# Kernel optimization log

Measured on AMD Instinct MI355X. Metric: run time of the kernel, lower is better.

## Reference

```python
import jax, jax.numpy as jnp
import numpy as np

EPS = 1e-16
S = 20  # amino-acid alphabet size, hardcoded in original (reshape to (-1,20,20))


def make_rate_matrix(R, p):
    """R: (n,S,S) symmetric, zero diag; p: (n,S) equilibrium. Returns normalized Q: (n,S,S)."""
    Q = R * p[:, None, :]
    diag = jnp.sum(Q, axis=-1, keepdims=True)          # (n,S,1)
    Q = Q - diag * jnp.eye(S, dtype=p.dtype)           # put -rowsum on diagonal
    mue = jnp.sum(p[..., None] * diag, axis=-2, keepdims=True)  # (n,1,1) expected mutation rate
    return Q / jnp.maximum(mue, EPS)


def setup_inputs() -> dict:
    key = jax.random.key(0)
    k1, k2, k3, k4, k5 = jax.random.split(key, 5)
    m, b, L, k, num_rates = 2, 512, 512, 2, 512
    sequences = jax.random.randint(k1, (m, b, L), 0, S, dtype=jnp.int32)
    rate_indices = jax.random.randint(k2, (m, b), 0, num_rates, dtype=jnp.int32)
    tau_kernel = jax.random.normal(k3, (m, num_rates), dtype=jnp.float32) - 3.0  # rate_init = const(-3)
    exchangeability_kernel = jax.random.normal(k4, (m, k, S, S), dtype=jnp.float32)
    equilibrium_kernel = jax.random.normal(k5, (m, k, S), dtype=jnp.float32)
    return {"sequences": sequences, "rate_indices": rate_indices, "tau_kernel": tau_kernel,
            "exchangeability_kernel": exchangeability_kernel, "equilibrium_kernel": equilibrium_kernel}


def reference(sequences, rate_indices, tau_kernel, exchangeability_kernel, equilibrium_kernel):
    m, k = exchangeability_kernel.shape[:2]
    b = sequences.shape[1]
    # make_R: symmetrize, softplus, zero diagonal
    R = jax.nn.softplus(0.5 * (exchangeability_kernel + jnp.swapaxes(exchangeability_kernel, -1, -2)))
    R = R * (1.0 - jnp.eye(S, dtype=R.dtype))
    # make_p: softmax equilibrium
    p = jax.nn.softmax(equilibrium_kernel, axis=-1)
    # normalized rate matrices Q: (m,k,S,S)
    Q = make_rate_matrix(R.reshape(-1, S, S), p.reshape(-1, S)).reshape(m, k, S, S)
    # make_tau: gather per-sequence time, softplus
    tau = jax.nn.softplus(tau_kernel[jnp.arange(m)[:, None], rate_indices])  # (m,b)
    # tau*Q and batched matrix exponential: (m,b,k,S,S)
    tauQ = tau[:, :, None, None, None] * Q[:, None]
    P = jax.scipy.linalg.expm(tauQ)
    # embedding-lookup combine: ancprobs[m,b,l,k,:] = P[m,b,k,seq[m,b,l],:]
    P_t = jnp.transpose(P, (0, 1, 3, 2, 4))  # (m,b,S,k,S)
    mi = jnp.arange(m)[:, None, None]
    bi = jnp.arange(b)[None, :, None]
    ancprobs = P_t[mi, bi, sequences]  # (m,b,L,k,S)
    return ancprobs
```

## Files before the change

kernel.cpp:

```cpp
#include <hip/hip_runtime.h>
#include <math.h>

#define SA 20
#define KDIM 2
#define MDIM 2
#define BDIM 512
#define LDIM 512
#define NRATES 512
#define PPB 4
#define THREADS 256
#define NCH (LDIM * KDIM * SA / 4)

__device__ __forceinline__ float softplusf(float x) {
    return fmaxf(x, 0.0f) + log1pf(expf(-fabsf(x)));
}

__device__ __forceinline__ void mmB(float* C, const float* A, const float* Bl) {
    #pragma unroll
    for (int j = 0; j < SA; ++j) C[j] = 0.0f;
    #pragma unroll
    for (int t = 0; t < SA; ++t) {
        const float a = A[t];
        const float4* row = reinterpret_cast<const float4*>(Bl + t * SA);
        #pragma unroll
        for (int q = 0; q < 5; ++q) {
            float4 b = row[q];
            C[4*q+0] = fmaf(a, b.x, C[4*q+0]);
            C[4*q+1] = fmaf(a, b.y, C[4*q+1]);
            C[4*q+2] = fmaf(a, b.z, C[4*q+2]);
            C[4*q+3] = fmaf(a, b.w, C[4*q+3]);
        }
    }
}

__device__ __forceinline__ void stageRow(float* dst, const float* T, int row, bool act) {
    if (act) {
        float4* d4 = reinterpret_cast<float4*>(dst + row * SA);
        #pragma unroll
        for (int q = 0; q < 5; ++q)
            d4[q] = make_float4(T[4*q+0], T[4*q+1], T[4*q+2], T[4*q+3]);
    }
}

__global__ __launch_bounds__(THREADS) void ancprobs_fused_kernel(
    const int*   __restrict__ seqg,
    const int*   __restrict__ rateIdx,
    const float* __restrict__ tauk,
    const float* __restrict__ Ek,
    const float* __restrict__ eqk,
    float*       __restrict__ out)
{
    __shared__ float sP[PPB * KDIM * SA * SA];
    __shared__ int   sSeq[PPB * LDIM];

    const int tid  = threadIdx.x;
    const int w    = tid >> 6;
    const int lane = tid & 63;
    const int mb   = blockIdx.x * PPB + w;
    const int mm   = mb >> 9;

    {
        const int4* sq = reinterpret_cast<const int4*>(seqg + (size_t)mb * LDIM);
        int4* dst = reinterpret_cast<int4*>(sSeq + w * LDIM);
        dst[lane]      = sq[lane];
        dst[lane + 64] = sq[lane + 64];
    }

    const int  half = lane >> 5;
    const int  row  = lane & 31;
    const bool act  = row < SA;
    const int  mk   = mm * KDIM + half;
    float* stage = sP + (w * KDIM + half) * SA * SA;

    float e = act ? eqk[mk * SA + row] : -INFINITY;
    float mx = e;
    #pragma unroll
    for (int off = 16; off; off >>= 1) mx = fmaxf(mx, __shfl_xor(mx, off, 32));
    float ex = act ? expf(e - mx) : 0.0f;
    float sm = ex;
    #pragma unroll
    for (int off = 16; off; off >>= 1) sm += __shfl_xor(sm, off, 32);
    float p_i = ex / sm;

    const int r0 = act ? row : 0;
    float A[SA];
    float dg = 0.0f;
    #pragma unroll
    for (int j = 0; j < SA; ++j) {
        float pj = __shfl(p_i, j, 32);
        float e1 = Ek[(mk * SA + r0) * SA + j];
        float e2 = Ek[(mk * SA + j) * SA + r0];
        float r  = (j == row) ? 0.0f : softplusf(0.5f * (e1 + e2));
        float q  = r * pj;
        A[j] = q;
        dg  += q;
    }
    float t_ = act ? p_i * dg : 0.0f;
    #pragma unroll
    for (int off = 16; off; off >>= 1) t_ += __shfl_xor(t_, off, 32);
    const float inv = 1.0f / fmaxf(t_, 1e-16f);

    const float tau = softplusf(tauk[mm * NRATES + rateIdx[mb]]);
    const float sc  = tau * inv;
    #pragma unroll
    for (int j = 0; j < SA; ++j)
        A[j] = act ? ((j == row) ? -dg * sc : A[j] * sc) : 0.0f;

    float rn = 0.0f;
    #pragma unroll
    for (int j = 0; j < SA; ++j) rn += fabsf(A[j]);
    #pragma unroll
    for (int off = 16; off; off >>= 1) rn = fmaxf(rn, __shfl_xor(rn, off, 32));
    int s = 0;
    if (rn > 1.0f) s = (int)ceilf(log2f(rn));
    if (s < 0) s = 0;
    if (s > 30) s = 30;
    const float scale = exp2f((float)(-s));
    #pragma unroll
    for (int j = 0; j < SA; ++j) A[j] *= scale;
    const int smax = max(s, __shfl_xor(s, 32, 64));

    float A2[SA], A3[SA], T[SA];
    stageRow(stage, A, row, act);
    mmB(A2, A, stage);
    mmB(A3, A2, stage);
    #pragma unroll
    for (int j = 0; j < SA; ++j) {
        float id = (j == row) ? 1.0f : 0.0f;
        T[j] = (1.0f/6.0f)*id + (1.0f/24.0f)*A[j] + (1.0f/120.0f)*A2[j] + (1.0f/720.0f)*A3[j];
    }
    stageRow(stage, T, row, act);
    {
        float P1[SA];
        mmB(P1, A3, stage);
        #pragma unroll
        for (int j = 0; j < SA; ++j) {
            float id = (j == row) ? 1.0f : 0.0f;
            T[j] = P1[j] + id + A[j] + 0.5f * A2[j];
        }
    }
    for (int it = 0; it < smax; ++it) {
        stageRow(stage, T, row, act);
        float Tn[SA];
        mmB(Tn, T, stage);
        const bool doit = it < s;
        #pragma unroll
        for (int j = 0; j < SA; ++j) T[j] = doit ? Tn[j] : T[j];
    }
    stageRow(stage, T, row, act);

    __syncthreads();

    const float4* pv = reinterpret_cast<const float4*>(sP);
    #pragma unroll 1
    for (int pr = 0; pr < PPB; ++pr) {
        float4* o4 = reinterpret_cast<float4*>(out) + (size_t)(blockIdx.x * PPB + pr) * NCH;
        const int* sq = sSeq + pr * LDIM;
        for (int f = tid; f < NCH; f += THREADS) {
            int l  = f / 10;
            int ch = f - l * 10;
            int kk = (ch >= 5) ? 1 : 0;
            int c4 = ch - kk * 5;
            o4[f] = pv[((pr * KDIM + kk) * SA + sq[l]) * 5 + c4];
        }
    }
}

extern "C" void kernel_launch(void* const* d_in, const int* in_sizes, int n_in,
                              void* d_out, int out_size, void* d_ws, size_t ws_size,
                              hipStream_t stream) {
    const int*   seq  = (const int*)d_in[0];
    const int*   ridx = (const int*)d_in[1];
    const float* tauk = (const float*)d_in[2];
    const float* Ek   = (const float*)d_in[3];
    const float* eqk  = (const float*)d_in[4];
    float* out = (float*)d_out;

    ancprobs_fused_kernel<<<(MDIM * BDIM) / PPB, THREADS, 0, stream>>>(
        seq, ridx, tauk, Ek, eqk, out);
}
```

Before: 109.8 us.

## Split fused kernel into expm kernel and wide gather kernel via workspace

```diff
diff --git a/kernel.cpp b/kernel.cpp
--- a/kernel.cpp
+++ b/kernel.cpp
@@ -7,9 +7,10 @@
 #define BDIM 512
 #define LDIM 512
 #define NRATES 512
-#define PPB 4
-#define THREADS 256
 #define NCH (LDIM * KDIM * SA / 4)
+#define GBLK_PER_PAIR 4
+#define GCHUNK (NCH / GBLK_PER_PAIR)
+#define GITER (GCHUNK / 256)
 
 __device__ __forceinline__ float softplusf(float x) {
     return fmaxf(x, 0.0f) + log1pf(expf(-fabsf(x)));
@@ -42,35 +43,24 @@
     }
 }
 
-__global__ __launch_bounds__(THREADS) void ancprobs_fused_kernel(
-    const int*   __restrict__ seqg,
+__global__ __launch_bounds__(64) void expm_kernel(
     const int*   __restrict__ rateIdx,
     const float* __restrict__ tauk,
     const float* __restrict__ Ek,
     const float* __restrict__ eqk,
-    float*       __restrict__ out)
+    float*       __restrict__ Pg)
 {
-    __shared__ float sP[PPB * KDIM * SA * SA];
-    __shared__ int   sSeq[PPB * LDIM];
+    __shared__ float sStage[KDIM * SA * SA];
 
-    const int tid  = threadIdx.x;
-    const int w    = tid >> 6;
-    const int lane = tid & 63;
-    const int mb   = blockIdx.x * PPB + w;
+    const int lane = threadIdx.x;
+    const int mb   = blockIdx.x;
     const int mm   = mb >> 9;
-
-    {
-        const int4* sq = reinterpret_cast<const int4*>(seqg + (size_t)mb * LDIM);
-        int4* dst = reinterpret_cast<int4*>(sSeq + w * LDIM);
-        dst[lane]      = sq[lane];
-        dst[lane + 64] = sq[lane + 64];
-    }
 
     const int  half = lane >> 5;
     const int  row  = lane & 31;
     const bool act  = row < SA;
     const int  mk   = mm * KDIM + half;
-    float* stage = sP + (w * KDIM + half) * SA * SA;
+    float* stage = sStage + half * SA * SA;
 
     float e = act ? eqk[mk * SA + row] : -INFINITY;
     float mx = e;
@@ -147,23 +137,47 @@
         #pragma unroll
         for (int j = 0; j < SA; ++j) T[j] = doit ? Tn[j] : T[j];
     }
-    stageRow(stage, T, row, act);
 
-    __syncthreads();
+    if (act) {
+        float4* d4 = reinterpret_cast<float4*>(Pg + ((size_t)mb * KDIM + half) * SA * SA + row * SA);
+        #pragma unroll
+        for (int q = 0; q < 5; ++q)
+            d4[q] = make_float4(T[4*q+0], T[4*q+1], T[4*q+2], T[4*q+3]);
+    }
+}
 
-    const float4* pv = reinterpret_cast<const float4*>(sP);
-    #pragma unroll 1
-    for (int pr = 0; pr < PPB; ++pr) {
-        float4* o4 = reinterpret_cast<float4*>(out) + (size_t)(blockIdx.x * PPB + pr) * NCH;
-        const int* sq = sSeq + pr * LDIM;
-        for (int f = tid; f < NCH; f += THREADS) {
-            int l  = f / 10;
-            int ch = f - l * 10;
-            int kk = (ch >= 5) ? 1 : 0;
-            int c4 = ch - kk * 5;
-            o4[f] = pv[((pr * KDIM + kk) * SA + sq[l]) * 5 + c4];
-        }
+__global__ __launch_bounds__(256) void gather_kernel(
+    const int*   __restrict__ seqg,
+    const float* __restrict__ Pg,
+    float*       __restrict__ out)
+{
+    const int tid   = threadIdx.x;
+    const int mb    = blockIdx.x >> 2;
+    const int cbase = (blockIdx.x & 3) * GCHUNK + tid;
+
+    const int*    sq = seqg + (size_t)mb * LDIM;
+    const float4* P4 = reinterpret_cast<const float4*>(Pg + (size_t)mb * KDIM * SA * SA);
+    float4*       o4 = reinterpret_cast<float4*>(out) + (size_t)mb * NCH;
+
+    int c[GITER], l[GITER], sqv[GITER], idx[GITER];
+    #pragma unroll
+    for (int i = 0; i < GITER; ++i) c[i] = cbase + i * 256;
+    #pragma unroll
+    for (int i = 0; i < GITER; ++i) l[i] = c[i] / 10;
+    #pragma unroll
+    for (int i = 0; i < GITER; ++i) sqv[i] = sq[l[i]];
+    #pragma unroll
+    for (int i = 0; i < GITER; ++i) {
+        int ch = c[i] - l[i] * 10;
+        int kk = (ch >= 5) ? 1 : 0;
+        int c4 = ch - kk * 5;
+        idx[i] = (kk * SA + sqv[i]) * 5 + c4;
     }
+    float4 v[GITER];
+    #pragma unroll
+    for (int i = 0; i < GITER; ++i) v[i] = P4[idx[i]];
+    #pragma unroll
+    for (int i = 0; i < GITER; ++i) o4[c[i]] = v[i];
 }
 
 extern "C" void kernel_launch(void* const* d_in, const int* in_sizes, int n_in,
@@ -175,7 +189,8 @@
     const float* Ek   = (const float*)d_in[3];
     const float* eqk  = (const float*)d_in[4];
     float* out = (float*)d_out;
+    float* Pg  = (float*)d_ws;
 
-    ancprobs_fused_kernel<<<(MDIM * BDIM) / PPB, THREADS, 0, stream>>>(
-        seq, ridx, tauk, Ek, eqk, out);
+    expm_kernel<<<MDIM * BDIM, 64, 0, stream>>>(ridx, tauk, Ek, eqk, Pg);
+    gather_kernel<<<MDIM * BDIM * GBLK_PER_PAIR, 256, 0, stream>>>(seq, Pg, out);
 }
```

New measurement: 121.0 us. 1.1x slower.

## Precompute Q powers once per model and split gather across four blocks per sequence

Applied to the files above, without the earlier changes.

```diff
diff --git a/kernel.cpp b/kernel.cpp
--- a/kernel.cpp
+++ b/kernel.cpp
@@ -7,9 +7,14 @@
 #define BDIM 512
 #define LDIM 512
 #define NRATES 512
-#define PPB 4
-#define THREADS 256
+#define NPOW 7
+#define MATW (SA * SA)
+#define PWSTRIDE (NPOW * MATW)
+#define SPLIT 4
 #define NCH (LDIM * KDIM * SA / 4)
+#define GCH (NCH / SPLIT)
+#define GITER (GCH / 256)
+#define LSLICE (LDIM / SPLIT)
 
 __device__ __forceinline__ float softplusf(float x) {
     return fmaxf(x, 0.0f) + log1pf(expf(-fabsf(x)));
@@ -42,35 +47,30 @@
     }
 }
 
-__global__ __launch_bounds__(THREADS) void ancprobs_fused_kernel(
-    const int*   __restrict__ seqg,
-    const int*   __restrict__ rateIdx,
-    const float* __restrict__ tauk,
+__device__ __forceinline__ void writeMat(float* base, const float* T, int row, bool act) {
+    if (act) {
+        float4* d4 = reinterpret_cast<float4*>(base + row * SA);
+        #pragma unroll
+        for (int q = 0; q < 5; ++q)
+            d4[q] = make_float4(T[4*q+0], T[4*q+1], T[4*q+2], T[4*q+3]);
+    }
+}
+
+__global__ __launch_bounds__(64) void powers_kernel(
     const float* __restrict__ Ek,
     const float* __restrict__ eqk,
-    float*       __restrict__ out)
+    float*       __restrict__ Pw,
+    float*       __restrict__ nInf)
 {
-    __shared__ float sP[PPB * KDIM * SA * SA];
-    __shared__ int   sSeq[PPB * LDIM];
-
-    const int tid  = threadIdx.x;
-    const int w    = tid >> 6;
-    const int lane = tid & 63;
-    const int mb   = blockIdx.x * PPB + w;
-    const int mm   = mb >> 9;
-
-    {
-        const int4* sq = reinterpret_cast<const int4*>(seqg + (size_t)mb * LDIM);
-        int4* dst = reinterpret_cast<int4*>(sSeq + w * LDIM);
-        dst[lane]      = sq[lane];
-        dst[lane + 64] = sq[lane + 64];
-    }
-
-    const int  half = lane >> 5;
-    const int  row  = lane & 31;
-    const bool act  = row < SA;
-    const int  mk   = mm * KDIM + half;
-    float* stage = sP + (w * KDIM + half) * SA * SA;
+    __shared__ float sB[KDIM * MATW];
+
+    const int lane = threadIdx.x;
+    const int mm   = blockIdx.x;
+    const int half = lane >> 5;
+    const int row  = lane & 31;
+    const bool act = row < SA;
+    const int mk   = mm * KDIM + half;
+    float* stg = sB + half * MATW;
 
     float e = act ? eqk[mk * SA + row] : -INFINITY;
     float mx = e;
@@ -83,7 +83,7 @@
     float p_i = ex / sm;
 
     const int r0 = act ? row : 0;
-    float A[SA];
+    float Q[SA];
     float dg = 0.0f;
     #pragma unroll
     for (int j = 0; j < SA; ++j) {
@@ -92,77 +92,160 @@
         float e2 = Ek[(mk * SA + j) * SA + r0];
         float r  = (j == row) ? 0.0f : softplusf(0.5f * (e1 + e2));
         float q  = r * pj;
-        A[j] = q;
+        Q[j] = q;
         dg  += q;
     }
     float t_ = act ? p_i * dg : 0.0f;
     #pragma unroll
     for (int off = 16; off; off >>= 1) t_ += __shfl_xor(t_, off, 32);
     const float inv = 1.0f / fmaxf(t_, 1e-16f);
-
-    const float tau = softplusf(tauk[mm * NRATES + rateIdx[mb]]);
-    const float sc  = tau * inv;
     #pragma unroll
     for (int j = 0; j < SA; ++j)
-        A[j] = act ? ((j == row) ? -dg * sc : A[j] * sc) : 0.0f;
+        Q[j] = act ? ((j == row) ? -dg * inv : Q[j] * inv) : 0.0f;
 
     float rn = 0.0f;
     #pragma unroll
-    for (int j = 0; j < SA; ++j) rn += fabsf(A[j]);
+    for (int j = 0; j < SA; ++j) rn += fabsf(Q[j]);
     #pragma unroll
     for (int off = 16; off; off >>= 1) rn = fmaxf(rn, __shfl_xor(rn, off, 32));
-    int s = 0;
-    if (rn > 1.0f) s = (int)ceilf(log2f(rn));
-    if (s < 0) s = 0;
-    if (s > 30) s = 30;
-    const float scale = exp2f((float)(-s));
-    #pragma unroll
-    for (int j = 0; j < SA; ++j) A[j] *= scale;
-    const int smax = max(s, __shfl_xor(s, 32, 64));
-
-    float A2[SA], A3[SA], T[SA];
-    stageRow(stage, A, row, act);
-    mmB(A2, A, stage);
-    mmB(A3, A2, stage);
-    #pragma unroll
-    for (int j = 0; j < SA; ++j) {
-        float id = (j == row) ? 1.0f : 0.0f;
-        T[j] = (1.0f/6.0f)*id + (1.0f/24.0f)*A[j] + (1.0f/120.0f)*A2[j] + (1.0f/720.0f)*A3[j];
-    }
-    stageRow(stage, T, row, act);
-    {
-        float P1[SA];
-        mmB(P1, A3, stage);
-        #pragma unroll
-        for (int j = 0; j < SA; ++j) {
-            float id = (j == row) ? 1.0f : 0.0f;
-            T[j] = P1[j] + id + A[j] + 0.5f * A2[j];
+    if (act && row == 0) nInf[mk] = rn;
+
+    float* base = Pw + (size_t)mk * PWSTRIDE;
+    if (act) {
+        float I[SA];
+        #pragma unroll
+        for (int j = 0; j < SA; ++j) I[j] = (j == row) ? 1.0f : 0.0f;
+        writeMat(base + 0 * MATW, I, row, act);
+    }
+    writeMat(base + 1 * MATW, Q, row, act);
+
+    stageRow(stg, Q, row, act);
+    __syncthreads();
+    float G2[SA], G3[SA];
+    mmB(G2, Q, stg);
+    writeMat(base + 2 * MATW, G2, row, act);
+    mmB(G3, G2, stg);
+    writeMat(base + 3 * MATW, G3, row, act);
+    __syncthreads();
+    stageRow(stg, G2, row, act);
+    __syncthreads();
+    {
+        float G4[SA];
+        mmB(G4, G2, stg);
+        writeMat(base + 4 * MATW, G4, row, act);
+    }
+    {
+        float G5[SA];
+        mmB(G5, G3, stg);
+        writeMat(base + 5 * MATW, G5, row, act);
+    }
+    __syncthreads();
+    stageRow(stg, G3, row, act);
+    __syncthreads();
+    {
+        float G6[SA];
+        mmB(G6, G3, stg);
+        writeMat(base + 6 * MATW, G6, row, act);
+    }
+}
+
+__global__ __launch_bounds__(256) void combo_gather_kernel(
+    const int*   __restrict__ seqg,
+    const int*   __restrict__ rateIdx,
+    const float* __restrict__ tauk,
+    const float* __restrict__ Pw,
+    const float* __restrict__ nInf,
+    float*       __restrict__ out)
+{
+    __shared__ float sPw[KDIM * PWSTRIDE];
+    __shared__ float sP[KDIM * MATW];
+    __shared__ int   sSeq[LSLICE];
+
+    const int tid = threadIdx.x;
+    const int mb  = blockIdx.x >> 2;
+    const int qq  = blockIdx.x & 3;
+    const int mm  = mb >> 9;
+
+    {
+        const float4* src = reinterpret_cast<const float4*>(Pw + (size_t)mm * KDIM * PWSTRIDE);
+        float4* dst = reinterpret_cast<float4*>(sPw);
+        for (int f = tid; f < KDIM * PWSTRIDE / 4; f += 256) dst[f] = src[f];
+    }
+    if (tid >= 64 && tid < 96) {
+        reinterpret_cast<int4*>(sSeq)[tid - 64] =
+            reinterpret_cast<const int4*>(seqg + (size_t)mb * LDIM)[qq * (LSLICE / 4) + (tid - 64)];
+    }
+    __syncthreads();
+
+    if (tid < 64) {
+        const int lane = tid;
+        const int half = lane >> 5;
+        const int row  = lane & 31;
+        const bool act = row < SA;
+        const int r0   = act ? row : 0;
+
+        const float tau = softplusf(tauk[mm * NRATES + rateIdx[mb]]);
+        const float n   = nInf[mm * KDIM + half];
+        float x0 = tau * n;
+        int s = 0;
+        if (x0 > 1.0f) s = (int)ceilf(log2f(x0));
+        if (s < 0) s = 0;
+        if (s > 30) s = 30;
+        const float x = tau * exp2f(-(float)s);
+
+        float cf[NPOW];
+        cf[0] = 1.0f;
+        cf[1] = x;
+        cf[2] = cf[1] * x * 0.5f;
+        cf[3] = cf[2] * x * (1.0f / 3.0f);
+        cf[4] = cf[3] * x * 0.25f;
+        cf[5] = cf[4] * x * 0.2f;
+        cf[6] = cf[5] * x * (1.0f / 6.0f);
+
+        float T[SA];
+        #pragma unroll
+        for (int j = 0; j < SA; ++j) T[j] = (j == row) ? 1.0f : 0.0f;
+        const float* pb = sPw + half * PWSTRIDE + r0 * SA;
+        #pragma unroll
+        for (int d = 1; d < NPOW; ++d) {
+            const float c = cf[d];
+            const float4* rp = reinterpret_cast<const float4*>(pb + d * MATW);
+            #pragma unroll
+            for (int q = 0; q < 5; ++q) {
+                float4 b = rp[q];
+                T[4*q+0] = fmaf(c, b.x, T[4*q+0]);
+                T[4*q+1] = fmaf(c, b.y, T[4*q+1]);
+                T[4*q+2] = fmaf(c, b.z, T[4*q+2]);
+                T[4*q+3] = fmaf(c, b.w, T[4*q+3]);
+            }
         }
-    }
-    for (int it = 0; it < smax; ++it) {
-        stageRow(stage, T, row, act);
-        float Tn[SA];
-        mmB(Tn, T, stage);
-        const bool doit = it < s;
-        #pragma unroll
-        for (int j = 0; j < SA; ++j) T[j] = doit ? Tn[j] : T[j];
-    }
-    stageRow(stage, T, row, act);
-
+
+        const int smax = max(s, __shfl_xor(s, 32));
+        float* stg = sP + half * MATW;
+        for (int it = 0; it < smax; ++it) {
+            stageRow(stg, T, row, act);
+            float Tn[SA];
+            mmB(Tn, T, stg);
+            const bool doit = it < s;
+            #pragma unroll
+            for (int j = 0; j < SA; ++j) T[j] = doit ? Tn[j] : T[j];
+        }
+        stageRow(stg, T, row, act);
+    }
     __syncthreads();
 
     const float4* pv = reinterpret_cast<const float4*>(sP);
-    #pragma unroll 1
-    for (int pr = 0; pr < PPB; ++pr) {
-        float4* o4 = reinterpret_cast<float4*>(out) + (size_t)(blockIdx.x * PPB + pr) * NCH;
-        const int* sq = sSeq + pr * LDIM;
-        for (int f = tid; f < NCH; f += THREADS) {
-            int l  = f / 10;
-            int ch = f - l * 10;
-            int kk = (ch >= 5) ? 1 : 0;
-            int c4 = ch - kk * 5;
-            o4[f] = pv[((pr * KDIM + kk) * SA + sq[l]) * 5 + c4];
-        }
+    float4* o4 = reinterpret_cast<float4*>(out) + (size_t)mb * NCH;
+    const int cb = qq * GCH + tid;
+    #pragma unroll
+    for (int i = 0; i < GITER; ++i) {
+        const int c  = cb + i * 256;
+        const int l  = c / 10;
+        const int ch = c - l * 10;
+        const int kk = (ch >= 5) ? 1 : 0;
+        const int c4 = ch - kk * 5;
+        const int sq = sSeq[l - qq * LSLICE];
+        o4[c] = pv[(kk * SA + sq) * 5 + c4];
     }
 }
 
@@ -174,8 +257,11 @@
     const float* tauk = (const float*)d_in[2];
     const float* Ek   = (const float*)d_in[3];
     const float* eqk  = (const float*)d_in[4];
-    float* out = (float*)d_out;
-
-    ancprobs_fused_kernel<<<(MDIM * BDIM) / PPB, THREADS, 0, stream>>>(
-        seq, ridx, tauk, Ek, eqk, out);
-}
+    float* out  = (float*)d_out;
+    float* Pw   = (float*)d_ws;
+    float* nInf = (float*)d_ws + MDIM * KDIM * PWSTRIDE;
+
+    powers_kernel<<<MDIM, 64, 0, stream>>>(Ek, eqk, Pw, nInf);
+    combo_gather_kernel<<<MDIM * BDIM * SPLIT, 256, 0, stream>>>(
+        seq, ridx, tauk, Pw, nInf, out);
+}
```

Measured after the change: 122.5 us. 1.12x slower.

## Precompute Q powers once per block and evaluate Taylor polynomial per tau

Applied to the files above, without the earlier changes.

```diff
diff --git a/kernel.cpp b/kernel.cpp
--- a/kernel.cpp
+++ b/kernel.cpp
@@ -7,8 +7,7 @@
 #define BDIM 512
 #define LDIM 512
 #define NRATES 512
-#define PPB 4
-#define THREADS 256
+#define MATW (SA * SA)
 #define NCH (LDIM * KDIM * SA / 4)
 
 __device__ __forceinline__ float softplusf(float x) {
@@ -42,7 +41,7 @@
     }
 }
 
-__global__ __launch_bounds__(THREADS) void ancprobs_fused_kernel(
+__global__ __launch_bounds__(256) void ancprobs_onepass_kernel(
     const int*   __restrict__ seqg,
     const int*   __restrict__ rateIdx,
     const float* __restrict__ tauk,
@@ -50,119 +49,188 @@
     const float* __restrict__ eqk,
     float*       __restrict__ out)
 {
-    __shared__ float sP[PPB * KDIM * SA * SA];
-    __shared__ int   sSeq[PPB * LDIM];
+    __shared__ __align__(16) float sPw[KDIM][6][MATW];
+    __shared__ __align__(16) float sT[2][KDIM][MATW];
+    __shared__ int   sSeq[LDIM];
+    __shared__ float sn[KDIM];
 
     const int tid  = threadIdx.x;
+    const int mb   = blockIdx.x;
+    const int mm   = mb >> 9;
     const int w    = tid >> 6;
     const int lane = tid & 63;
-    const int mb   = blockIdx.x * PPB + w;
-    const int mm   = mb >> 9;
-
+
+    const int   ri  = rateIdx[mb];
+    const float tau = softplusf(tauk[mm * NRATES + ri]);
+
+    if (tid < 128)
+        reinterpret_cast<int4*>(sSeq)[tid] =
+            reinterpret_cast<const int4*>(seqg + (size_t)mb * LDIM)[tid];
+
+    if (w == 0) {
+        const int  half = lane >> 5;
+        const int  row  = lane & 31;
+        const bool act  = row < SA;
+        const int  mk   = mm * KDIM + half;
+        const int  r0   = act ? row : 0;
+
+        float e = act ? eqk[mk * SA + row] : -INFINITY;
+        float mx = e;
+        #pragma unroll
+        for (int off = 16; off; off >>= 1) mx = fmaxf(mx, __shfl_xor(mx, off, 32));
+        float ex = act ? expf(e - mx) : 0.0f;
+        float sm = ex;
+        #pragma unroll
+        for (int off = 16; off; off >>= 1) sm += __shfl_xor(sm, off, 32);
+        float p_i = ex / sm;
+
+        float Q[SA];
+        float dg = 0.0f;
+        #pragma unroll
+        for (int j = 0; j < SA; ++j) {
+            float pj = __shfl(p_i, j, 32);
+            float e1 = Ek[(mk * SA + r0) * SA + j];
+            float e2 = Ek[(mk * SA + j) * SA + r0];
+            float r  = (j == row) ? 0.0f : softplusf(0.5f * (e1 + e2));
+            float q  = r * pj;
+            Q[j] = q;
+            dg  += q;
+        }
+        float t_ = act ? p_i * dg : 0.0f;
+        #pragma unroll
+        for (int off = 16; off; off >>= 1) t_ += __shfl_xor(t_, off, 32);
+        const float inv = 1.0f / fmaxf(t_, 1e-16f);
+        #pragma unroll
+        for (int j = 0; j < SA; ++j)
+            Q[j] = act ? ((j == row) ? -dg * inv : Q[j] * inv) : 0.0f;
+
+        float rn = 0.0f;
+        #pragma unroll
+        for (int j = 0; j < SA; ++j) rn += fabsf(Q[j]);
+        #pragma unroll
+        for (int off = 16; off; off >>= 1) rn = fmaxf(rn, __shfl_xor(rn, off, 32));
+        if (act && row == 0) sn[half] = rn;
+
+        stageRow(&sPw[half][0][0], Q, row, act);
+        float G2[SA];
+        mmB(G2, Q, &sPw[half][0][0]);
+        stageRow(&sPw[half][1][0], G2, row, act);
+        float G3[SA];
+        mmB(G3, G2, &sPw[half][0][0]);
+        stageRow(&sPw[half][2][0], G3, row, act);
+    }
+    __syncthreads();
+
+    if (w >= 1) {
+        const int  half = lane >> 5;
+        const int  row  = lane & 31;
+        const bool act  = row < SA;
+        const int  r0   = act ? row : 0;
+        const int  srcA = (w == 1) ? 1 : 2;
+        const int  srcB = (w == 3) ? 2 : 1;
+        const int  dst  = w + 2;
+
+        float A[SA];
+        const float4* a4 = reinterpret_cast<const float4*>(&sPw[half][srcA][0] + r0 * SA);
+        #pragma unroll
+        for (int q = 0; q < 5; ++q) {
+            float4 v = a4[q];
+            A[4*q+0] = v.x; A[4*q+1] = v.y; A[4*q+2] = v.z; A[4*q+3] = v.w;
+        }
+        float G[SA];
+        mmB(G, A, &sPw[half][srcB][0]);
+        stageRow(&sPw[half][dst][0], G, row, act);
+    }
+    __syncthreads();
+
+    const float n0 = sn[0], n1 = sn[1];
+    int s0 = 0, s1 = 0;
     {
-        const int4* sq = reinterpret_cast<const int4*>(seqg + (size_t)mb * LDIM);
-        int4* dst = reinterpret_cast<int4*>(sSeq + w * LDIM);
-        dst[lane]      = sq[lane];
-        dst[lane + 64] = sq[lane + 64];
-    }
-
-    const int  half = lane >> 5;
-    const int  row  = lane & 31;
-    const bool act  = row < SA;
-    const int  mk   = mm * KDIM + half;
-    float* stage = sP + (w * KDIM + half) * SA * SA;
-
-    float e = act ? eqk[mk * SA + row] : -INFINITY;
-    float mx = e;
+        float y0 = tau * n0;
+        if (y0 > 1.0f) s0 = (int)ceilf(log2f(y0));
+        s0 = min(max(s0, 0), 30);
+        float y1 = tau * n1;
+        if (y1 > 1.0f) s1 = (int)ceilf(log2f(y1));
+        s1 = min(max(s1, 0), 30);
+    }
+    float cf0[6], cf1[6];
+    {
+        float x = tau * exp2f(-(float)s0);
+        cf0[0] = x;             cf0[1] = cf0[0] * x * 0.5f;
+        cf0[2] = cf0[1] * x * (1.0f/3.0f); cf0[3] = cf0[2] * x * 0.25f;
+        cf0[4] = cf0[3] * x * 0.2f;        cf0[5] = cf0[4] * x * (1.0f/6.0f);
+        x = tau * exp2f(-(float)s1);
+        cf1[0] = x;             cf1[1] = cf1[0] * x * 0.5f;
+        cf1[2] = cf1[1] * x * (1.0f/3.0f); cf1[3] = cf1[2] * x * 0.25f;
+        cf1[4] = cf1[3] * x * 0.2f;        cf1[5] = cf1[4] * x * (1.0f/6.0f);
+    }
+
     #pragma unroll
-    for (int off = 16; off; off >>= 1) mx = fmaxf(mx, __shfl_xor(mx, off, 32));
-    float ex = act ? expf(e - mx) : 0.0f;
-    float sm = ex;
-    #pragma unroll
-    for (int off = 16; off; off >>= 1) sm += __shfl_xor(sm, off, 32);
-    float p_i = ex / sm;
-
-    const int r0 = act ? row : 0;
-    float A[SA];
-    float dg = 0.0f;
-    #pragma unroll
-    for (int j = 0; j < SA; ++j) {
-        float pj = __shfl(p_i, j, 32);
-        float e1 = Ek[(mk * SA + r0) * SA + j];
-        float e2 = Ek[(mk * SA + j) * SA + r0];
-        float r  = (j == row) ? 0.0f : softplusf(0.5f * (e1 + e2));
-        float q  = r * pj;
-        A[j] = q;
-        dg  += q;
-    }
-    float t_ = act ? p_i * dg : 0.0f;
-    #pragma unroll
-    for (int off = 16; off; off >>= 1) t_ += __shfl_xor(t_, off, 32);
-    const float inv = 1.0f / fmaxf(t_, 1e-16f);
-
-    const float tau = softplusf(tauk[mm * NRATES + rateIdx[mb]]);
-    const float sc  = tau * inv;
-    #pragma unroll
-    for (int j = 0; j < SA; ++j)
-        A[j] = act ? ((j == row) ? -dg * sc : A[j] * sc) : 0.0f;
-
-    float rn = 0.0f;
-    #pragma unroll
-    for (int j = 0; j < SA; ++j) rn += fabsf(A[j]);
-    #pragma unroll
-    for (int off = 16; off; off >>= 1) rn = fmaxf(rn, __shfl_xor(rn, off, 32));
-    int s = 0;
-    if (rn > 1.0f) s = (int)ceilf(log2f(rn));
-    if (s < 0) s = 0;
-    if (s > 30) s = 30;
-    const float scale = exp2f((float)(-s));
-    #pragma unroll
-    for (int j = 0; j < SA; ++j) A[j] *= scale;
-    const int smax = max(s, __shfl_xor(s, 32, 64));
-
-    float A2[SA], A3[SA], T[SA];
-    stageRow(stage, A, row, act);
-    mmB(A2, A, stage);
-    mmB(A3, A2, stage);
-    #pragma unroll
-    for (int j = 0; j < SA; ++j) {
-        float id = (j == row) ? 1.0f : 0.0f;
-        T[j] = (1.0f/6.0f)*id + (1.0f/24.0f)*A[j] + (1.0f/120.0f)*A2[j] + (1.0f/720.0f)*A3[j];
-    }
-    stageRow(stage, T, row, act);
-    {
-        float P1[SA];
-        mmB(P1, A3, stage);
-        #pragma unroll
-        for (int j = 0; j < SA; ++j) {
-            float id = (j == row) ? 1.0f : 0.0f;
-            T[j] = P1[j] + id + A[j] + 0.5f * A2[j];
-        }
-    }
-    for (int it = 0; it < smax; ++it) {
-        stageRow(stage, T, row, act);
-        float Tn[SA];
-        mmB(Tn, T, stage);
-        const bool doit = it < s;
-        #pragma unroll
-        for (int j = 0; j < SA; ++j) T[j] = doit ? Tn[j] : T[j];
-    }
-    stageRow(stage, T, row, act);
-
+    for (int ei = 0; ei < 4; ++ei) {
+        const int e = tid + ei * 256;
+        if (ei < 3 || tid < 32) {
+            const int kk  = (e >= MATW) ? 1 : 0;
+            const int idx = e - kk * MATW;
+            const float* cf = kk ? cf1 : cf0;
+            float acc = (idx % 21 == 0) ? 1.0f : 0.0f;
+            #pragma unroll
+            for (int d = 0; d < 6; ++d)
+                acc = fmaf(cf[d], sPw[kk][d][idx], acc);
+            sT[0][kk][idx] = acc;
+        }
+    }
     __syncthreads();
 
-    const float4* pv = reinterpret_cast<const float4*>(sP);
+    int buf = 0;
+    const int smax = max(s0, s1);
+    if (smax > 0) {
+        for (int it = 0; it < smax; ++it) {
+            #pragma unroll
+            for (int ei = 0; ei < 4; ++ei) {
+                const int e = tid + ei * 256;
+                if (ei < 3 || tid < 32) {
+                    const int kk  = (e >= MATW) ? 1 : 0;
+                    const int idx = e - kk * MATW;
+                    const int r   = idx / SA;
+                    const int c   = idx - r * SA;
+                    const int sk  = kk ? s1 : s0;
+                    float acc;
+                    if (it < sk) {
+                        acc = 0.0f;
+                        const float* Tm = &sT[buf][kk][0];
+                        #pragma unroll
+                        for (int t = 0; t < SA; ++t)
+                            acc = fmaf(Tm[r * SA + t], Tm[t * SA + c], acc);
+                    } else {
+                        acc = sT[buf][kk][idx];
+                    }
+                    sT[buf ^ 1][kk][idx] = acc;
+                }
+            }
+            __syncthreads();
+            buf ^= 1;
+        }
+    }
+
+    const float4* pv = reinterpret_cast<const float4*>(&sT[buf][0][0]);
+    float4* o4 = reinterpret_cast<float4*>(out) + (size_t)mb * NCH;
     #pragma unroll 1
-    for (int pr = 0; pr < PPB; ++pr) {
-        float4* o4 = reinterpret_cast<float4*>(out) + (size_t)(blockIdx.x * PPB + pr) * NCH;
-        const int* sq = sSeq + pr * LDIM;
-        for (int f = tid; f < NCH; f += THREADS) {
-            int l  = f / 10;
-            int ch = f - l * 10;
-            int kk = (ch >= 5) ? 1 : 0;
-            int c4 = ch - kk * 5;
-            o4[f] = pv[((pr * KDIM + kk) * SA + sq[l]) * 5 + c4];
-        }
+    for (int g = 0; g < 4; ++g) {
+        int    cc[5];
+        float4 v[5];
+        #pragma unroll
+        for (int i = 0; i < 5; ++i) {
+            const int c  = tid + (g * 5 + i) * 256;
+            const int l  = c / 10;
+            const int ch = c - l * 10;
+            const int kk = (ch >= 5) ? 1 : 0;
+            const int c4 = ch - kk * 5;
+            const int sq = sSeq[l];
+            cc[i] = c;
+            v[i]  = pv[kk * 100 + sq * 5 + c4];
+        }
+        #pragma unroll
+        for (int i = 0; i < 5; ++i) o4[cc[i]] = v[i];
     }
 }
 
@@ -176,6 +244,6 @@
     const float* eqk  = (const float*)d_in[4];
     float* out = (float*)d_out;
 
-    ancprobs_fused_kernel<<<(MDIM * BDIM) / PPB, THREADS, 0, stream>>>(
+    ancprobs_onepass_kernel<<<MDIM * BDIM, 256, 0, stream>>>(
         seq, ridx, tauk, Ek, eqk, out);
 }
```

Result: slower. 158.1 us (+44.0%).
